# Performance work log

Hardware: AMD Instinct MI355X
Metric: run time of the kernel (lower is better)

Reference implementation:

```python
import jax, jax.numpy as jnp
import numpy as np

B, S, HID = 2, 1024, 4096
NH, NKV, HD = 32, 8, 128
EPS = 1e-6
ROPE_THETA = 1000000.0
SCALE = HD ** -0.5
NREP = NH // NKV


def _rope_tables(batch, seq, head_dim, theta):
    inv_freq = 1.0 / (theta ** (np.arange(0, head_dim, 2, dtype=np.float32) / head_dim))
    pos = np.arange(seq, dtype=np.float32)
    freqs = np.outer(pos, inv_freq)            # [S, HD/2]
    emb = np.concatenate([freqs, freqs], -1)   # [S, HD]
    cos = np.broadcast_to(np.cos(emb), (batch, seq, head_dim))
    sin = np.broadcast_to(np.sin(emb), (batch, seq, head_dim))
    return jnp.asarray(cos), jnp.asarray(sin)


def setup_inputs() -> dict:
    key = jax.random.key(0)
    k1, k2, k3 = jax.random.split(key, 3)
    hidden_states = jax.random.normal(k1, (B, S, HID), dtype=jnp.float32)
    cos, sin = _rope_tables(B, S, HD, ROPE_THETA)
    attention_mask = jnp.ones((B, 1, S, S), dtype=bool)
    w_qkv = jax.random.normal(k2, ((NH + 2 * NKV) * HD, HID), dtype=jnp.float32) * (HID ** -0.5)
    w_q_norm = jnp.ones((HD,), dtype=jnp.float32)
    w_k_norm = jnp.ones((HD,), dtype=jnp.float32)
    w_o = jax.random.normal(k3, (HID, NH * HD), dtype=jnp.float32) * ((NH * HD) ** -0.5)
    return {"hidden_states": hidden_states, "cos": cos, "sin": sin,
            "attention_mask": attention_mask, "w_qkv": w_qkv,
            "w_q_norm": w_q_norm, "w_k_norm": w_k_norm, "w_o": w_o}


def _rms_norm(x, w):
    var = jnp.mean(jnp.square(x), axis=-1, keepdims=True)
    return x * jax.lax.rsqrt(var + EPS) * w


def _rotate_half(x):
    x1, x2 = jnp.split(x, 2, axis=-1)
    return jnp.concatenate([-x2, x1], axis=-1)


def reference(hidden_states, cos, sin, attention_mask, w_qkv, w_q_norm, w_k_norm, w_o):
    qkv = jnp.einsum('bsh,oh->bso', hidden_states, w_qkv)  # [B,S,(NH+2NKV)*HD]
    q, k, v = jnp.split(qkv, [NH * HD, (NH + NKV) * HD], axis=-1)
    q = _rms_norm(q.reshape(B, S, NH, HD), w_q_norm).transpose(0, 2, 1, 3)   # [B,NH,S,HD]
    k = _rms_norm(k.reshape(B, S, NKV, HD), w_k_norm).transpose(0, 2, 1, 3)  # [B,NKV,S,HD]
    v = v.reshape(B, S, NKV, HD).transpose(0, 2, 1, 3)                        # [B,NKV,S,HD]
    c = cos[:, None, :, :]
    s = sin[:, None, :, :]
    q = q * c + _rotate_half(q) * s
    k = k * c + _rotate_half(k) * s
    k = jnp.repeat(k, NREP, axis=1)  # GQA repeat -> [B,NH,S,HD]
    v = jnp.repeat(v, NREP, axis=1)
    scores = jnp.einsum('bhqd,bhkd->bhqk', q, k) * SCALE
    scores = jnp.where(attention_mask, scores, jnp.finfo(scores.dtype).min)
    attn = jax.nn.softmax(scores, axis=-1)
    out = jnp.einsum('bhqk,bhkd->bhqd', attn, v)
    out = out.transpose(0, 2, 1, 3).reshape(B, S, NH * HD)
    return jnp.einsum('bsd,od->bso', out, w_o)
```

## Files before the change

kernel.cpp:

```cpp
#include <hip/hip_runtime.h>
#include <hip/hip_bf16.h>

typedef __bf16 bf16_t;
typedef bf16_t bf16x2 __attribute__((ext_vector_type(2)));
typedef bf16_t bf16x8 __attribute__((ext_vector_type(8)));
typedef float f32x4 __attribute__((ext_vector_type(4)));

#define DEVI __device__ __forceinline__

DEVI void gld_lds16(const void* g, void* l) {
  __builtin_amdgcn_global_load_lds(
      (const __attribute__((address_space(1))) void*)g,
      (__attribute__((address_space(3))) void*)l, 16, 0, 0);
}

DEVI bf16x8 cvt8(f32x4 a, f32x4 b) {
  return bf16x8{(__bf16)a[0], (__bf16)a[1], (__bf16)a[2], (__bf16)a[3],
                (__bf16)b[0], (__bf16)b[1], (__bf16)b[2], (__bf16)b[3]};
}

__global__ __launch_bounds__(256) void cvt_f32_bf16(
    const float* __restrict__ in, bf16_t* __restrict__ out, long n) {
  long i = ((long)blockIdx.x * 256 + threadIdx.x) * 8;
  if (i >= n) return;
  float4 a = *(const float4*)(in + i);
  float4 b = *(const float4*)(in + i + 4);
  bf16x8 v = {(__bf16)a.x, (__bf16)a.y, (__bf16)a.z, (__bf16)a.w,
              (__bf16)b.x, (__bf16)b.y, (__bf16)b.z, (__bf16)b.w};
  *(bf16x8*)(out + i) = v;
}

template <typename CT>
__global__ __launch_bounds__(512, 4) void gemmf(
    const bf16_t* __restrict__ Ab, const float* __restrict__ Wf,
    CT* __restrict__ C, int M, int N, int K) {
  constexpr int FC = 2;
  __shared__ __align__(16) bf16_t As[2][128 * 64];
  __shared__ __align__(16) bf16_t Bs[2][128 * 64];
  const int tid = threadIdx.x, wave = tid >> 6, lane = tid & 63;
  const int q16 = lane & 15, gq = lane >> 4, sw = q16 & 7;
  const int wm = wave >> 2, wn = wave & 3;
  const int nM = M >> 7, nN = N >> 7;
  const int cM = nM >> 1, cN = nN >> 2;
  const int xcd = (int)blockIdx.x & 7, wi = (int)blockIdx.x >> 3;
  const int tm = ((xcd >> 2) * cM + wi / cN) << 7;
  const int tn = ((xcd & 3) * cN + wi % cN) << 7;
  const int NT = K >> 6;
  const bf16_t* Ag = Ab + (size_t)tm * K;
  const float* Wg = Wf + (size_t)tn * K;
  const int sr = (wave << 3) + (lane >> 3);
  const int c8 = (lane & 7) * 8;
  const int swz8 = (((lane & 7) ^ (sr & 7)) << 3);
  const int ldsoff = sr * 64 + swz8;

#define BISSUE(kq, rg)                                             \
  {                                                                \
    _Pragma("unroll") for (int u = 0; u < FC; ++u) {               \
      const float* p = Wg + (size_t)(u * 64 + sr) * K + (kq) + c8; \
      rg[u][0] = *(const f32x4*)p;                                 \
      rg[u][1] = *(const f32x4*)(p + 4);                           \
    }                                                              \
  }
#define WRU(base, u, rg) \
  *(bf16x8*)(&(base)[0] + (u)*4096 + ldsoff) = cvt8(rg[u][0], rg[u][1]);
#define AGLD(kq, buf)                                           \
  {                                                             \
    _Pragma("unroll") for (int u = 0; u < 2; ++u)               \
        gld_lds16(Ag + (size_t)(u * 64 + sr) * K + (kq) + swz8, \
                  &As[buf][0] + u * 4096 + (wave << 9));        \
  }

  f32x4 acc[4][FC];
#pragma unroll
  for (int i = 0; i < 4; ++i)
#pragma unroll
    for (int j = 0; j < FC; ++j) acc[i][j] = f32x4{0.f, 0.f, 0.f, 0.f};

  f32x4 brg[FC][2];

  AGLD(0, 0);
  AGLD(64, 1);
  BISSUE(0, brg);
  asm volatile("s_waitcnt vmcnt(0)" ::: "memory");
#pragma unroll
  for (int u = 0; u < FC; ++u) WRU(Bs[0], u, brg);
  asm volatile("s_waitcnt lgkmcnt(0)" ::: "memory");
  __builtin_amdgcn_s_barrier();

  for (int t = 0; t < NT; ++t) {
    const int cur = t & 1;
    const bf16_t* Acur = As[cur];
    const bf16_t* Bcur = Bs[cur];
    const int k1 = (t + 1) << 6, k2 = (t + 2) << 6;
    bf16x8 afr[4][2];

    if (t + 1 < NT) BISSUE(k1, brg);
    __builtin_amdgcn_sched_barrier(0);
#pragma unroll
    for (int fr = 0; fr < 4; ++fr) {
      const bf16_t* rp = Acur + (wm * 64 + fr * 16 + q16) * 64;
      afr[fr][0] = *(const bf16x8*)(rp + ((gq ^ sw) << 3));
      afr[fr][1] = *(const bf16x8*)(rp + (((4 + gq) ^ sw) << 3));
    }
    bf16x8 b1[2];
    {
      const bf16_t* rp = Bcur + (wn * 32 + q16) * 64;
      b1[0] = *(const bf16x8*)(rp + ((gq ^ sw) << 3));
      b1[1] = *(const bf16x8*)(rp + (((4 + gq) ^ sw) << 3));
    }
    __builtin_amdgcn_s_barrier();

    __builtin_amdgcn_s_setprio(1);
#pragma unroll
    for (int fr = 0; fr < 4; ++fr)
#pragma unroll
      for (int kk = 0; kk < 2; ++kk)
        acc[fr][0] = __builtin_amdgcn_mfma_f32_16x16x32_bf16(
            afr[fr][kk], b1[kk], acc[fr][0], 0, 0, 0);
    __builtin_amdgcn_s_setprio(0);
    __builtin_amdgcn_sched_barrier(0);
    asm volatile("s_waitcnt vmcnt(0)" ::: "memory");
    if (t + 1 < NT) {
#pragma unroll
      for (int u = 0; u < FC; ++u) WRU(Bs[cur ^ 1], u, brg);
    }
    if (t + 2 < NT) AGLD(k2, cur);

    bf16x8 b2[2];
    {
      const bf16_t* rp = Bcur + (wn * 32 + 16 + q16) * 64;
      b2[0] = *(const bf16x8*)(rp + ((gq ^ sw) << 3));
      b2[1] = *(const bf16x8*)(rp + (((4 + gq) ^ sw) << 3));
    }
    __builtin_amdgcn_s_setprio(1);
#pragma unroll
    for (int fr = 0; fr < 4; ++fr)
#pragma unroll
      for (int kk = 0; kk < 2; ++kk)
        acc[fr][1] = __builtin_amdgcn_mfma_f32_16x16x32_bf16(
            afr[fr][kk], b2[kk], acc[fr][1], 0, 0, 0);
    __builtin_amdgcn_s_setprio(0);
    asm volatile("s_waitcnt lgkmcnt(0)" ::: "memory");
    __builtin_amdgcn_s_barrier();
  }

#pragma unroll
  for (int fr = 0; fr < 4; ++fr)
#pragma unroll
    for (int fc = 0; fc < FC; ++fc)
#pragma unroll
      for (int i = 0; i < 4; ++i) {
        int row = tm + wm * 64 + fr * 16 + gq * 4 + i;
        int col = tn + wn * 32 + fc * 16 + q16;
        C[(size_t)row * N + col] = (CT)acc[fr][fc][i];
      }
#undef BISSUE
#undef WRU
#undef AGLD
}

__global__ __launch_bounds__(256) void rope_scatter(
    const bf16_t* __restrict__ qkv, const float* __restrict__ cosb,
    const float* __restrict__ sinb, const float* __restrict__ wq,
    const float* __restrict__ wk, bf16_t* __restrict__ qb,
    bf16_t* __restrict__ kb, bf16_t* __restrict__ vt) {
  const int row = blockIdx.x;
  const int b = row >> 10, s = row & 1023;
  const int wave = threadIdx.x >> 6, lane = threadIdx.x & 63;
  const int d0 = 2 * lane;
  const float c0 = cosb[(size_t)row * 128 + d0];
  const float c1 = cosb[(size_t)row * 128 + d0 + 1];
  const float s0 = sinb[(size_t)row * 128 + d0];
  const float s1 = sinb[(size_t)row * 128 + d0 + 1];
  const float g0q = wq[d0], g1q = wq[d0 + 1];
  const float g0k = wk[d0], g1k = wk[d0 + 1];
  const float sign = (lane < 32) ? -1.f : 1.f;

  for (int h = wave; h < 32; h += 4) {
    const bf16_t* x = qkv + (size_t)row * 6144 + h * 128 + d0;
    float x0 = (float)x[0], x1 = (float)x[1];
    float ss = x0 * x0 + x1 * x1;
#pragma unroll
    for (int off = 1; off < 64; off <<= 1) ss += __shfl_xor(ss, off);
    float r = rsqrtf(ss * (1.0f / 128.0f) + 1e-6f);
    float n0 = x0 * r * g0q, n1 = x1 * r * g1q;
    float o0 = __shfl_xor(n0, 32), o1 = __shfl_xor(n1, 32);
    float y0 = n0 * c0 + sign * o0 * s0;
    float y1 = n1 * c1 + sign * o1 * s1;
    bf16_t* dst = qb + ((size_t)(b * 32 + h) * 1024 + s) * 128 + d0;
    dst[0] = (__bf16)y0;
    dst[1] = (__bf16)y1;
  }
  for (int h = wave; h < 8; h += 4) {
    const bf16_t* x = qkv + (size_t)row * 6144 + 4096 + h * 128 + d0;
    float x0 = (float)x[0], x1 = (float)x[1];
    float ss = x0 * x0 + x1 * x1;
#pragma unroll
    for (int off = 1; off < 64; off <<= 1) ss += __shfl_xor(ss, off);
    float r = rsqrtf(ss * (1.0f / 128.0f) + 1e-6f);
    float n0 = x0 * r * g0k, n1 = x1 * r * g1k;
    float o0 = __shfl_xor(n0, 32), o1 = __shfl_xor(n1, 32);
    float y0 = n0 * c0 + sign * o0 * s0;
    float y1 = n1 * c1 + sign * o1 * s1;
    bf16_t* dst = kb + ((size_t)(b * 8 + h) * 1024 + s) * 128 + d0;
    dst[0] = (__bf16)y0;
    dst[1] = (__bf16)y1;
  }
  for (int h = wave; h < 8; h += 4) {
    const bf16_t* x = qkv + (size_t)row * 6144 + 5120 + h * 128 + d0;
    bf16_t* dst = vt + ((size_t)(b * 8 + h) * 128 + d0) * 1024 + s;
    dst[0] = x[0];
    dst[1024] = x[1];
  }
}

__global__ __launch_bounds__(256, 2) void attn_fwd(
    const bf16_t* __restrict__ Qb, const bf16_t* __restrict__ Kb,
    const bf16_t* __restrict__ Vt, bf16_t* __restrict__ Ob) {
  __shared__ __align__(16) bf16_t Kl[2][64 * 128];
  __shared__ __align__(16) bf16_t Vl[2][128 * 64];
  __shared__ __align__(16) bf16_t Pl[4][32 * 64];
  const int tid = threadIdx.x, wave = tid >> 6, lane = tid & 63;
  const int q16 = lane & 15, g = lane >> 4;
  const int bid = blockIdx.x;
  const int bh = bid >> 3, qt = bid & 7;
  const int b = bh >> 5, h = bh & 31;
  const int kvh = (b << 3) + (h >> 2);
  const bf16_t* qp = Qb + ((size_t)bh * 1024 + qt * 128 + wave * 32) * 128;
  const bf16_t* kp = Kb + (size_t)kvh * (1024 * 128);
  const bf16_t* vp = Vt + (size_t)kvh * (128 * 1024);
  const float SCALE = 0.088388347648318447f;
  const int sw = q16 & 7;

  bf16x8 qf[2][4];
#pragma unroll
  for (int m = 0; m < 2; ++m)
#pragma unroll
    for (int kc = 0; kc < 4; ++kc)
      qf[m][kc] = *(const bf16x8*)(qp + (m * 16 + q16) * 128 + kc * 32 + g * 8);

  f32x4 oacc[2][8];
#pragma unroll
  for (int m = 0; m < 2; ++m)
#pragma unroll
    for (int dc = 0; dc < 8; ++dc) oacc[m][dc] = f32x4{0.f, 0.f, 0.f, 0.f};
  float m_run[2] = {-3.0e38f, -3.0e38f}, l_run[2] = {0.f, 0.f};

#define STAGE_KV(buf, jj)                                                      \
  {                                                                            \
    _Pragma("unroll") for (int i = 0; i < 4; ++i) {                            \
      int n = (wave * 4 + i) * 64 + lane;                                      \
      int rk = n >> 4, ck = (n & 15) ^ (rk & 7);                               \
      gld_lds16(kp + (size_t)((jj) + rk) * 128 + ck * 8,                       \
                &Kl[buf][0] + (wave * 4 + i) * 512);                           \
      int rv = n >> 3, cv = (n & 7) ^ (rv & 7);                                \
      gld_lds16(vp + (size_t)rv * 1024 + (jj) + cv * 8,                        \
                &Vl[buf][0] + (wave * 4 + i) * 512);                           \
    }                                                                          \
  }

  STAGE_KV(0, 0);
  __syncthreads();
  int cur = 0;

  for (int jt = 0; jt < 16; ++jt) {
    if (jt < 15) STAGE_KV(cur ^ 1, (jt + 1) * 64);

    const bf16_t* Kc = &Kl[cur][0];
    const bf16_t* Vc = &Vl[cur][0];
    bf16_t* Plw = &Pl[wave][0];

    f32x4 st[2][4];
#pragma unroll
    for (int m = 0; m < 2; ++m)
#pragma unroll
      for (int t = 0; t < 4; ++t) st[m][t] = f32x4{0.f, 0.f, 0.f, 0.f};
#pragma unroll
    for (int t = 0; t < 4; ++t) {
      bf16x8 kf[4];
#pragma unroll
      for (int kc = 0; kc < 4; ++kc)
        kf[kc] = *(const bf16x8*)(Kc + (t * 16 + q16) * 128 + (((kc * 4 + g) ^ sw) << 3));
#pragma unroll
      for (int m = 0; m < 2; ++m)
#pragma unroll
        for (int kc = 0; kc < 4; ++kc)
          st[m][t] = __builtin_amdgcn_mfma_f32_16x16x32_bf16(kf[kc], qf[m][kc], st[m][t], 0, 0, 0);
    }

#pragma unroll
    for (int m = 0; m < 2; ++m) {
      float mx = m_run[m];
#pragma unroll
      for (int t = 0; t < 4; ++t)
#pragma unroll
        for (int i = 0; i < 4; ++i) {
          float s = st[m][t][i] * SCALE;
          st[m][t][i] = s;
          mx = fmaxf(mx, s);
        }
      mx = fmaxf(mx, __shfl_xor(mx, 16));
      mx = fmaxf(mx, __shfl_xor(mx, 32));
      float alpha = __expf(m_run[m] - mx);
      float lsum = 0.f;
      const int prow = m * 16 + q16;
#pragma unroll
      for (int t = 0; t < 4; ++t) {
        float p0 = __expf(st[m][t][0] - mx);
        float p1 = __expf(st[m][t][1] - mx);
        float p2 = __expf(st[m][t][2] - mx);
        float p3 = __expf(st[m][t][3] - mx);
        lsum += (p0 + p1) + (p2 + p3);
        int k0 = t * 16 + g * 4;
        int a0 = prow * 64 + ((((k0 >> 3)) ^ sw) << 3) + (k0 & 7);
        *(bf16x2*)(Plw + a0) = bf16x2{(__bf16)p0, (__bf16)p1};
        *(bf16x2*)(Plw + a0 + 2) = bf16x2{(__bf16)p2, (__bf16)p3};
      }
      lsum += __shfl_xor(lsum, 16);
      lsum += __shfl_xor(lsum, 32);
      l_run[m] = l_run[m] * alpha + lsum;
      m_run[m] = mx;
      float ar[4];
#pragma unroll
      for (int i = 0; i < 4; ++i) ar[i] = __shfl(alpha, g * 4 + i);
#pragma unroll
      for (int dc = 0; dc < 8; ++dc)
#pragma unroll
        for (int i = 0; i < 4; ++i) oacc[m][dc][i] *= ar[i];
    }

#pragma unroll
    for (int ks = 0; ks < 2; ++ks) {
      bf16x8 pf0 = *(const bf16x8*)(Plw + (q16)*64 + (((ks * 4 + g) ^ sw) << 3));
      bf16x8 pf1 = *(const bf16x8*)(Plw + (16 + q16) * 64 + (((ks * 4 + g) ^ sw) << 3));
#pragma unroll
      for (int dc = 0; dc < 8; ++dc) {
        bf16x8 vf = *(const bf16x8*)(Vc + (dc * 16 + q16) * 64 + (((ks * 4 + g) ^ sw) << 3));
        oacc[0][dc] = __builtin_amdgcn_mfma_f32_16x16x32_bf16(pf0, vf, oacc[0][dc], 0, 0, 0);
        oacc[1][dc] = __builtin_amdgcn_mfma_f32_16x16x32_bf16(pf1, vf, oacc[1][dc], 0, 0, 0);
      }
    }

    __syncthreads();
    cur ^= 1;
  }

  const int rowbase = (b << 10) + qt * 128 + wave * 32;
#pragma unroll
  for (int m = 0; m < 2; ++m) {
    float lr[4];
#pragma unroll
    for (int i = 0; i < 4; ++i) lr[i] = __shfl(l_run[m], g * 4 + i);
#pragma unroll
    for (int dc = 0; dc < 8; ++dc)
#pragma unroll
      for (int i = 0; i < 4; ++i) {
        int row = rowbase + m * 16 + g * 4 + i;
        int col = (h << 7) + dc * 16 + q16;
        Ob[(size_t)row * 4096 + col] = (__bf16)(oacc[m][dc][i] / lr[i]);
      }
  }
#undef STAGE_KV
}

extern "C" void kernel_launch(void* const* d_in, const int* in_sizes, int n_in,
                              void* d_out, int out_size, void* d_ws,
                              size_t ws_size, hipStream_t stream) {
  const float* hidden = (const float*)d_in[0];
  const float* cosb = (const float*)d_in[1];
  const float* sinb = (const float*)d_in[2];
  const float* w_qkv = (const float*)d_in[4];
  const float* w_qn = (const float*)d_in[5];
  const float* w_kn = (const float*)d_in[6];
  const float* w_o = (const float*)d_in[7];
  float* out = (float*)d_out;

  char* ws = (char*)d_ws;
  bf16_t* hb = (bf16_t*)ws;
  bf16_t* qkv = (bf16_t*)(ws + 16777216);
  bf16_t* qb = (bf16_t*)(ws + 41943040);
  bf16_t* kb = (bf16_t*)(ws + 58720256);
  bf16_t* vt = (bf16_t*)(ws + 62914560);
  bf16_t* attno = (bf16_t*)(ws + 67108864);

  cvt_f32_bf16<<<dim3(4096), dim3(256), 0, stream>>>(hidden, hb, 8388608);
  gemmf<bf16_t><<<dim3(768), dim3(512), 0, stream>>>(hb, w_qkv, qkv, 2048, 6144, 4096);
  rope_scatter<<<dim3(2048), dim3(256), 0, stream>>>(qkv, cosb, sinb, w_qn, w_kn, qb, kb, vt);
  attn_fwd<<<dim3(64 * 8), dim3(256), 0, stream>>>(qb, kb, vt, attno);
  gemmf<float><<<dim3(512), dim3(512), 0, stream>>>(attno, w_o, out, 2048, 4096, 4096);
}
```

Measured before the change: 330.5 us.

## Pre-convert QKV weights to bf16 and use async-LDS bf16 GEMM with 128x192 tiles

Adds a separate pass that converts the fp32 w_qkv matrix to bf16 in workspace, then runs a new bf16×bf16 GEMM that loads both operands into LDS with global_load_lds. Each block computes a 128x192 tile in a two-phase pipeline per K step, so the grid is 512 blocks instead of 768. The aim is to stop converting fp32 weights inside the GEMM loop and to get more reuse per block. In exchange it adds a full read of the fp32 weight matrix and a write of its bf16 copy every call, and the workspace buffers are reshuffled so several of them alias.

```diff
diff --git a/kernel.cpp b/kernel.cpp
--- a/kernel.cpp
+++ b/kernel.cpp
@@ -28,6 +28,127 @@
   bf16x8 v = {(__bf16)a.x, (__bf16)a.y, (__bf16)a.z, (__bf16)a.w,
               (__bf16)b.x, (__bf16)b.y, (__bf16)b.z, (__bf16)b.w};
   *(bf16x8*)(out + i) = v;
+}
+
+template <int FC, int MINW, typename CT>
+__global__ __launch_bounds__(512, MINW) void gemm128(
+    const bf16_t* __restrict__ A, const bf16_t* __restrict__ W,
+    CT* __restrict__ C, int M, int N, int K) {
+  constexpr int BN = FC * 64;
+  constexpr int P1 = FC / 2, P2 = FC - P1;
+  __shared__ __align__(16) bf16_t As[2][128 * 64];
+  __shared__ __align__(16) bf16_t Bs[2][BN * 64];
+  const int tid = threadIdx.x, wave = tid >> 6, lane = tid & 63;
+  const int q16 = lane & 15, gq = lane >> 4, sw = q16 & 7;
+  const int wm = wave >> 2, wn = wave & 3;
+  const int nM = M >> 7, nN = N / BN;
+  const int cM = nM >> 1, cN = nN >> 2;
+  const int xcd = (int)blockIdx.x & 7, wi = (int)blockIdx.x >> 3;
+  const int tm = ((xcd >> 2) * cM + wi / cN) << 7;
+  const int tn = ((xcd & 3) * cN + wi % cN) * BN;
+  const int NT = K >> 6;
+  const bf16_t* Ag = A + (size_t)tm * K;
+  const bf16_t* Wg = W + (size_t)tn * K;
+  const int sr = (wave << 3) + (lane >> 3);
+  const int scol = (((lane & 7) ^ (sr & 7)) << 3);
+
+#define STG(gbase, kq, uu, ldsbuf)                              \
+  gld_lds16((gbase) + (size_t)((uu)*64 + sr) * K + (kq) + scol, \
+            &(ldsbuf)[0] + (uu)*4096 + (wave << 9))
+
+  f32x4 acc[4][FC];
+#pragma unroll
+  for (int i = 0; i < 4; ++i)
+#pragma unroll
+    for (int j = 0; j < FC; ++j) acc[i][j] = f32x4{0.f, 0.f, 0.f, 0.f};
+
+  STG(Ag, 0, 0, As[0]);
+  STG(Ag, 0, 1, As[0]);
+#pragma unroll
+  for (int u = 0; u < FC; ++u) STG(Wg, 0, u, Bs[0]);
+  STG(Ag, 64, 0, As[1]);
+  STG(Ag, 64, 1, As[1]);
+  asm volatile("s_waitcnt vmcnt(2)" ::: "memory");
+  __builtin_amdgcn_s_barrier();
+
+  for (int t = 0; t < NT; ++t) {
+    const int cur = t & 1;
+    const bf16_t* Acur = As[cur];
+    const bf16_t* Bcur = Bs[cur];
+    const int k1 = (t + 1) << 6, k2 = (t + 2) << 6;
+    bf16x8 afr[4][2];
+
+#pragma unroll
+    for (int fr = 0; fr < 4; ++fr) {
+      const bf16_t* rp = Acur + (wm * 64 + fr * 16 + q16) * 64;
+      afr[fr][0] = *(const bf16x8*)(rp + ((gq ^ sw) << 3));
+      afr[fr][1] = *(const bf16x8*)(rp + (((4 + gq) ^ sw) << 3));
+    }
+    bf16x8 b1[P1][2];
+#pragma unroll
+    for (int fc = 0; fc < P1; ++fc) {
+      const bf16_t* rp = Bcur + (wn * (16 * FC) + fc * 16 + q16) * 64;
+      b1[fc][0] = *(const bf16x8*)(rp + ((gq ^ sw) << 3));
+      b1[fc][1] = *(const bf16x8*)(rp + (((4 + gq) ^ sw) << 3));
+    }
+    if (t + 1 < NT) {
+#pragma unroll
+      for (int u = 0; u < FC; ++u) STG(Wg, k1, u, Bs[cur ^ 1]);
+    }
+    __builtin_amdgcn_s_barrier();
+    __builtin_amdgcn_s_setprio(1);
+#pragma unroll
+    for (int fr = 0; fr < 4; ++fr)
+#pragma unroll
+      for (int fc = 0; fc < P1; ++fc)
+#pragma unroll
+        for (int kk = 0; kk < 2; ++kk)
+          acc[fr][fc] = __builtin_amdgcn_mfma_f32_16x16x32_bf16(
+              afr[fr][kk], b1[fc][kk], acc[fr][fc], 0, 0, 0);
+    __builtin_amdgcn_s_setprio(0);
+    asm volatile("" ::: "memory");
+    __builtin_amdgcn_s_barrier();
+
+    bf16x8 b2[P2][2];
+#pragma unroll
+    for (int f2 = 0; f2 < P2; ++f2) {
+      const bf16_t* rp = Bcur + (wn * (16 * FC) + (P1 + f2) * 16 + q16) * 64;
+      b2[f2][0] = *(const bf16x8*)(rp + ((gq ^ sw) << 3));
+      b2[f2][1] = *(const bf16x8*)(rp + (((4 + gq) ^ sw) << 3));
+    }
+    if (t + 2 < NT) {
+      STG(Ag, k2, 0, As[cur]);
+      STG(Ag, k2, 1, As[cur]);
+    }
+    __builtin_amdgcn_s_barrier();
+    __builtin_amdgcn_s_setprio(1);
+#pragma unroll
+    for (int fr = 0; fr < 4; ++fr)
+#pragma unroll
+      for (int f2 = 0; f2 < P2; ++f2)
+#pragma unroll
+        for (int kk = 0; kk < 2; ++kk)
+          acc[fr][P1 + f2] = __builtin_amdgcn_mfma_f32_16x16x32_bf16(
+              afr[fr][kk], b2[f2][kk], acc[fr][P1 + f2], 0, 0, 0);
+    __builtin_amdgcn_s_setprio(0);
+    if (t + 2 < NT)
+      asm volatile("s_waitcnt vmcnt(2)" ::: "memory");
+    else
+      asm volatile("s_waitcnt vmcnt(0)" ::: "memory");
+    __builtin_amdgcn_s_barrier();
+  }
+
+#pragma unroll
+  for (int fr = 0; fr < 4; ++fr)
+#pragma unroll
+    for (int fc = 0; fc < FC; ++fc)
+#pragma unroll
+      for (int i = 0; i < 4; ++i) {
+        int row = tm + wm * 64 + fr * 16 + gq * 4 + i;
+        int col = tn + wn * (16 * FC) + fc * 16 + q16;
+        C[(size_t)row * N + col] = (CT)acc[fr][fc][i];
+      }
+#undef STG
 }
 
 template <typename CT>
@@ -376,15 +497,17 @@
   float* out = (float*)d_out;
 
   char* ws = (char*)d_ws;
-  bf16_t* hb = (bf16_t*)ws;
-  bf16_t* qkv = (bf16_t*)(ws + 16777216);
-  bf16_t* qb = (bf16_t*)(ws + 41943040);
-  bf16_t* kb = (bf16_t*)(ws + 58720256);
-  bf16_t* vt = (bf16_t*)(ws + 62914560);
-  bf16_t* attno = (bf16_t*)(ws + 67108864);
+  bf16_t* wqkvb = (bf16_t*)ws;
+  bf16_t* qb = (bf16_t*)ws;
+  bf16_t* kb = (bf16_t*)(ws + 16777216);
+  bf16_t* vt = (bf16_t*)(ws + 20971520);
+  bf16_t* hb = (bf16_t*)(ws + 50331648);
+  bf16_t* attno = hb;
+  bf16_t* qkv = (bf16_t*)(ws + 67108864);
 
   cvt_f32_bf16<<<dim3(4096), dim3(256), 0, stream>>>(hidden, hb, 8388608);
-  gemmf<bf16_t><<<dim3(768), dim3(512), 0, stream>>>(hb, w_qkv, qkv, 2048, 6144, 4096);
+  cvt_f32_bf16<<<dim3(12288), dim3(256), 0, stream>>>(w_qkv, wqkvb, 25165824);
+  gemm128<3, 4, bf16_t><<<dim3(512), dim3(512), 0, stream>>>(hb, wqkvb, qkv, 2048, 6144, 4096);
   rope_scatter<<<dim3(2048), dim3(256), 0, stream>>>(qkv, cosb, sinb, w_qn, w_kn, qb, kb, vt);
   attn_fwd<<<dim3(64 * 8), dim3(256), 0, stream>>>(qb, kb, vt, attno);
   gemmf<float><<<dim3(512), dim3(512), 0, stream>>>(attno, w_o, out, 2048, 4096, 4096);
```

Measured after the change: 290.9 us. -12.0%, faster.
